# Performance work log

Hardware: AMD Instinct MI355X
Metric: run time of the kernel (lower is better)

The kernel has to match this reference:

```python
import jax, jax.numpy as jnp
import numpy as np

MC = 16384
IND_T = 96
N_MAT = 4
N_STRIKES = 21


def _init_linear(key, fan_in, fan_out, prefix=()):
    k1, k2 = jax.random.split(key)
    lim = 1.0 / np.sqrt(fan_in)
    W = jax.random.uniform(k1, prefix + (fan_in, fan_out), minval=-lim, maxval=lim, dtype=jnp.float32)
    b = jax.random.uniform(k2, prefix + (fan_out,), minval=-lim, maxval=lim, dtype=jnp.float32)
    return W, b


def setup_inputs() -> dict:
    key = jax.random.key(0)
    ks = jax.random.split(key, 14)
    z = jax.random.normal(ks[0], (MC, IND_T), dtype=jnp.float32)
    zz = jax.random.normal(ks[1], (MC, IND_T), dtype=jnp.float32)
    timegrid = jnp.arange(IND_T + 1, dtype=jnp.float32) / 365.0  # daily grid
    maturities = jnp.array([24, 48, 72, 96], dtype=jnp.int32)    # in days
    strikes = jnp.linspace(0.8, 1.2, N_STRIKES, dtype=jnp.float32)
    sv_W1, sv_b1 = _init_linear(ks[2], 3, 100)
    sv_W2, sv_b2 = _init_linear(ks[3], 100, 100)
    sv_W3, sv_b3 = _init_linear(ks[4], 100, 1)
    vh_W1, vh_b1 = _init_linear(ks[5], 2, 20, (N_MAT,))
    vh_W2, vh_b2 = _init_linear(ks[6], 20, N_STRIKES, (N_MAT,))
    vd_W1, vd_b1 = _init_linear(ks[7], 1, 20)
    vd_W2, vd_b2 = _init_linear(ks[8], 20, 1)
    vv_W1, vv_b1 = _init_linear(ks[9], 1, 20)
    vv_W2, vv_b2 = _init_linear(ks[10], 20, 1)
    v0 = jax.random.uniform(ks[11], (1,), dtype=jnp.float32) * 0.1
    rho = jnp.ones((1,), dtype=jnp.float32) * -2.0
    return dict(S0=jnp.float32(1.0), rate=jnp.float32(0.05), z=z, zz=zz,
                timegrid=timegrid, strikes=strikes, v0=v0, rho=rho,
                sv_W1=sv_W1, sv_b1=sv_b1, sv_W2=sv_W2, sv_b2=sv_b2, sv_W3=sv_W3, sv_b3=sv_b3,
                vh_W1=vh_W1, vh_b1=vh_b1, vh_W2=vh_W2, vh_b2=vh_b2,
                vd_W1=vd_W1, vd_b1=vd_b1, vd_W2=vd_W2, vd_b2=vd_b2,
                vv_W1=vv_W1, vv_b1=vv_b1, vv_W2=vv_W2, vv_b2=vv_b2,
                maturities=maturities)


def reference(S0, rate, z, zz, timegrid, strikes, v0, rho,
              sv_W1, sv_b1, sv_W2, sv_b2, sv_W3, sv_b3,
              vh_W1, vh_b1, vh_W2, vh_b2,
              vd_W1, vd_b1, vd_W2, vd_b2,
              vv_W1, vv_b1, vv_W2, vv_b2,
              maturities):
    sg = jax.lax.stop_gradient
    mc = z.shape[0]
    n_mat = vh_W1.shape[0]
    n_strikes = strikes.shape[0]

    def s_vol(x):  # [MC,3] -> [MC,1], softplus output
        h1 = jax.nn.relu(x @ sv_W1 + sv_b1)
        h2 = jax.nn.relu(h1 @ sv_W2 + sv_b2)
        return jax.nn.softplus(h2 @ sv_W3 + sv_b3)

    def v_drift(v):  # [MC,1] -> [MC,1]
        return jax.nn.relu(v @ vd_W1 + vd_b1) @ vd_W2 + vd_b2

    def v_vol(v):  # [MC,1] -> [MC,1], softplus output
        return jax.nn.softplus(jax.nn.relu(v @ vv_W1 + vv_b1) @ vv_W2 + vv_b2)

    def vanilla_hedge_all(x):  # [MC,2] -> [MC, n_strikes, n_mat] (one net per maturity)
        h1 = jax.nn.relu(jnp.einsum('mi,kio->kmo', x, vh_W1) + vh_b1[:, None, :])
        out = jax.nn.softplus(jnp.einsum('kmo,koj->kmj', h1, vh_W2) + vh_b2[:, None, :])
        return jnp.transpose(out, (1, 2, 0))

    rho_t = jnp.tanh(rho)[0]
    days = jnp.round(timegrid * 365.0).astype(jnp.int32)       # [IND_T+1]
    le = days[1:, None] <= maturities[None, :]                  # [IND_T, n_mat]
    idx_net = jnp.argmax(le, axis=1)                            # first live maturity per step
    is_mat = jnp.any(days[1:, None] == maturities[None, :], axis=1)
    mat_idx = jnp.arange(n_mat)

    Slog0 = jnp.log(jnp.full((mc, 1), S0, dtype=jnp.float32))
    V0 = jnp.full((mc, 1), 1.0, dtype=jnp.float32) * jax.nn.sigmoid(v0)[0] * 0.5
    cv0 = jnp.zeros((mc, n_strikes, n_mat), dtype=jnp.float32)
    pv0 = jnp.zeros((n_mat, n_strikes), dtype=jnp.float32)

    xs = (z.T[:, :, None], zz.T[:, :, None], timegrid[:-1], timegrid[1:], idx_net, is_mat)

    def step(carry, x):
        Slog_old, V_old, cv, pv_h, pv_var = carry
        z_i, zz_i, t0, t1, idx, im = x
        h = t1 - t0
        sqh = jnp.sqrt(h)
        dW = sqh * z_i                                          # [MC,1]
        dB = rho_t * dW + jnp.sqrt(1.0 - rho_t ** 2) * sqh * zz_i
        ones_t = jnp.full((mc, 1), 1.0, dtype=jnp.float32) * t0
        pd = s_vol(jnp.concatenate([ones_t, Slog_old, V_old], axis=1))  # price diffusion
        cv_fwd = vanilla_hedge_all(jnp.concatenate([ones_t, sg(Slog_old)], axis=1))
        V_new = V_old + v_drift(V_old) * h + v_vol(V_old) * dB
        drift = rate - 0.5 * pd ** 2
        diff = pd * dW
        drift_c = 1.0 + jnp.abs(sg(drift)) * sqh                # tamed Euler
        diff_c = 1.0 + jnp.abs(sg(pd)) * sqh
        Slog_new = Slog_old + drift * h / drift_c + diff / diff_c
        S_new = jnp.exp(Slog_new)
        S_old = jnp.exp(Slog_old)
        dS = jnp.exp(-rate * t1) * S_new - jnp.exp(-rate * t0) * S_old  # [MC,1]
        mask = (mat_idx >= idx).astype(cv.dtype)                # live maturities only
        cv = cv + mask[None, None, :] * cv_fwd * sg(dS)[:, :, None]
        # hedged vanilla (call) prices collected at maturity steps
        payoff = jnp.exp(-rate * t1) * jnp.maximum(S_new - strikes[None, :], 0.0)
        price = payoff - cv[:, :, idx]                          # [MC, n_strikes]
        pv = jnp.mean(price, axis=0)
        pvar = jnp.var(price, axis=0, ddof=1)
        sel = (mat_idx == idx)[:, None] & im
        pv_h = jnp.where(sel, pv[None, :], pv_h)
        pv_var = jnp.where(sel, pvar[None, :], pv_var)
        return (Slog_new, V_new, cv, pv_h, pv_var), None

    (_, _, _, pv_h, pv_var), _ = jax.lax.scan(step, (Slog0, V0, cv0, pv0, pv0), xs)
    return jnp.stack([pv_h, pv_var])  # [2, n_mat, n_strikes]
```

## Files before the change

kernel.cpp:

```cpp
#include <hip/hip_runtime.h>
#include <hip/hip_bf16.h>
#include <math.h>


#define MC      16384
#define NSTEP   96
#define BLOCK   512
#define NGROUP  512
#define NPAIR   84

typedef short bf16x8 __attribute__((ext_vector_type(8)));
typedef float f32x4  __attribute__((ext_vector_type(4)));

union U8 { uint4 u; bf16x8 v; };
union BF2U { __hip_bfloat162 b; unsigned u; };

__device__ __forceinline__ unsigned bf16rne(float x) {
    unsigned u = __float_as_uint(x);
    return (u + 0x7FFFu + ((u >> 16) & 1u)) >> 16;
}
__device__ __forceinline__ unsigned pk2(float lo, float hi) {
    BF2U t; t.b = __float22bfloat162_rn(make_float2(lo, hi));
    return t.u;
}
__device__ __forceinline__ float sp(float x) {
    return fmaxf(x, 0.f) + __logf(1.f + __expf(-fabsf(x)));
}

__global__ __launch_bounds__(BLOCK, 4)
void lsv_sim(const float* __restrict__ S0p,   const float* __restrict__ ratep,
             const float* __restrict__ z,     const float* __restrict__ zzg,
             const float* __restrict__ strikesg,
             const float* __restrict__ v0p,   const float* __restrict__ rhop,
             const float* __restrict__ svW1,  const float* __restrict__ svb1,
             const float* __restrict__ svW2,  const float* __restrict__ svb2,
             const float* __restrict__ svW3,  const float* __restrict__ svb3,
             const float* __restrict__ vhW1,  const float* __restrict__ vhb1,
             const float* __restrict__ vhW2,  const float* __restrict__ vhb2,
             const float* __restrict__ vdW1,  const float* __restrict__ vdb1,
             const float* __restrict__ vdW2,  const float* __restrict__ vdb2,
             const float* __restrict__ vvW1,  const float* __restrict__ vvb1,
             const float* __restrict__ vvW2,  const float* __restrict__ vvb2,
             const int*   __restrict__ mats,
             float* __restrict__ psum, float* __restrict__ psq)
{
    __shared__ __align__(16) unsigned short H1c[16 * 32 * 8];
    __shared__ __align__(16) float W1f[16 * 32];
    __shared__ __align__(16) float WH1f[16 * 32];
    __shared__ __align__(16) float B2T[128], W3T[128];
    __shared__ __align__(16) float RED[32 * 4];
    __shared__ float VDl[32], VVl[32];
    __shared__ float PSs[2][32], PSq[2][32];
    __shared__ __align__(16) float VW[128];
    __shared__ __align__(16) float4 STEP[NSTEP];
    __shared__ float D1T[NSTEP];
    __shared__ int   ITAB[NSTEP];
    __shared__ float ZT[32][97], ZZT[32][97];
    __shared__ float SLOG[32], VST[32], SST[32], SLOGP[32], DSP[32];
    __shared__ __align__(16) float CW1[2][128];
    __shared__ __align__(16) float CH[2][128];

    const int tid  = threadIdx.x;
    const int lane = tid & 63;
    const int w    = __builtin_amdgcn_readfirstlane(tid >> 6);
    const int quad = lane >> 4;
    const int col  = lane & 15;
    const int lp   = lane & 31;

    const int pt = w & 1;
    const int jg = w >> 1;
    const int hm = w >> 1;

    {
        const size_t gbase = (size_t)blockIdx.x * 32 * NSTEP;
        for (int e = tid; e < 32 * NSTEP; e += BLOCK) {
            const int p = e / NSTEP, ii = e - p * NSTEP;
            ZT[p][ii]  = z  [gbase + e];
            ZZT[p][ii] = zzg[gbase + e];
        }
    }
    for (int e = tid; e < 128; e += BLOCK) {
        float v = 0.f;
        if      (e < 20)             v = vdW1[e];
        else if (e < 40)             v = vdb1[e - 20];
        else if (e < 60)             v = vdW2[e - 40];
        else if (e >= 64 && e < 84)  v = vvW1[e - 64];
        else if (e >= 84 && e < 104) v = vvb1[e - 84];
        else if (e >= 104 && e < 124)v = vvW2[e - 104];
        else if (e == 124)           v = vdb2[0];
        else if (e == 125)           v = vvb2[0];
        VW[e] = v;
        B2T[e] = (e < 100) ? svb2[e] : 0.f;
        W3T[e] = (e < 100) ? svW3[e] : 0.f;
    }
    for (int e = tid; e < 512; e += BLOCK) {
        const int kc2 = e >> 5, r5 = e & 31, grp = r5 >> 3, kk = kc2 * 8 + (r5 & 7);
        float v = 0.f;
        if (kk < 100) v = (grp == 0) ? svW1[kk] : (grp == 1) ? svW1[100 + kk]
                        : (grp == 2) ? svW1[200 + kk] : svb1[kk];
        W1f[e] = v;
    }
    for (int e = tid; e < 512; e += BLOCK) {
        const int hq = e >> 5, r5 = e & 31, grp = r5 >> 3;
        const int hmm = hq >> 2, qq = hq & 3;
        const int j = qq * 8 + (r5 & 7);
        float v = 0.f;
        if (j < 20 && grp < 3)
            v = (grp == 0) ? vhW1[hmm * 40 + j] : (grp == 1) ? vhW1[hmm * 40 + 20 + j]
                                                : vhb1[hmm * 20 + j];
        WH1f[e] = v;
    }

    const float rate  = ratep[0];
    const float S0    = S0p[0];
    const float rho_t = tanhf(rhop[0]);
    const float srho  = sqrtf(1.f - rho_t * rho_t);
    const float b3    = svb3[0];

    if (tid < NSTEP) {
        const int i = tid;
        const float t0 = (float)i       * (1.f / 365.f);
        const float t1 = (float)(i + 1) * (1.f / 365.f);
        const float h  = t1 - t0;
        STEP[i] = make_float4(t0, h, sqrtf(h), __expf(-rate * t0));
        D1T[i]  = __expf(-rate * t1);
        const int day = i + 1;
        const int m0 = mats[0], m1 = mats[1], m2 = mats[2], m3 = mats[3];
        const int idx = (day > m0) + (day > m1) + (day > m2);
        const int mi  = (idx == 0) ? m0 : (idx == 1) ? m1 : (idx == 2) ? m2 : m3;
        ITAB[i] = idx | ((day == mi) ? 256 : 0);
    }

    bf16x8 Af[4][2];
#pragma unroll
    for (int c = 0; c < 4; c++)
#pragma unroll
        for (int t = 0; t < 2; t++) {
            U8 tt;
#pragma unroll
            for (int e2 = 0; e2 < 4; e2++) {
                const int k0 = 32 * c + 8 * quad + 2 * e2;
                const int j  = (2 * jg + t) * 16 + col;
                const float v0 = (k0     < 100 && j < 100) ? svW2[k0 * 100 + j]       : 0.f;
                const float v1 = (k0 + 1 < 100 && j < 100) ? svW2[(k0 + 1) * 100 + j] : 0.f;
                (&tt.u.x)[e2] = bf16rne(v0) | (bf16rne(v1) << 16);
            }
            Af[c][t] = tt.v;
        }
    bf16x8 Ah[2];
#pragma unroll
    for (int st = 0; st < 2; st++) {
        U8 tt;
#pragma unroll
        for (int e2 = 0; e2 < 4; e2++) {
            const int j0 = 8 * quad + 2 * e2, j1 = j0 + 1;
            const int s  = st * 16 + col;
            const float v0 = (j0 < 20 && s < 21) ? vhW2[hm * 420 + j0 * 21 + s] : 0.f;
            const float v1 = (j1 < 20 && s < 21) ? vhW2[hm * 420 + j1 * 21 + s] : 0.f;
            (&tt.u.x)[e2] = bf16rne(v0) | (bf16rne(v1) << 16);
        }
        Ah[st] = tt.v;
    }
    f32x4 c0h, c1h;
    float K0a[4], K1a[4];
#pragma unroll
    for (int r = 0; r < 4; r++) {
        const int s0 = quad * 4 + r, s1 = 16 + quad * 4 + r;
        c0h[r] = vhb2[hm * 21 + s0];
        K0a[r] = strikesg[s0];
        c1h[r] = (s1 < 21) ? vhb2[hm * 21 + s1] : 0.f;
        K1a[r] = (s1 < 21) ? strikesg[s1] : 1e30f;
    }

    float Slog = __logf(S0);
    float S    = __expf(Slog);
    float V    = (1.f / (1.f + __expf(-v0p[0]))) * 0.5f;
    f32x4 cv0 = {0.f, 0.f, 0.f, 0.f};
    f32x4 cv1 = {0.f, 0.f, 0.f, 0.f};

    const int path = pt * 16 + col;
    const int kc   = jg * 4 + quad;

    __syncthreads();

    if (tid < 128) {
        const float t00 = STEP[0].x;
        const int kk = tid;
        CW1[0][kk] = fmaf(t00, W1f[(kk >> 3) * 32 + (kk & 7)],
                               W1f[(kk >> 3) * 32 + 24 + (kk & 7)]);
    } else if (tid < 256) {
        const float t00 = STEP[0].x;
        const int e = tid - 128;
        CH[0][e] = fmaf(t00, WH1f[(e >> 3) * 32 + (e & 7)],
                             WH1f[(e >> 3) * 32 + 16 + (e & 7)]);
    }
    if (tid < 32) {
        SLOG[tid] = Slog;
        SST[tid]  = S;
        VST[tid]  = V;
    }

    __syncthreads();

    const int j0e = (2 * jg) * 16 + quad * 4;
    const float4 b2a = *reinterpret_cast<const float4*>(B2T + j0e);
    const float4 w3a = *reinterpret_cast<const float4*>(W3T + j0e);
    const float4 b2b = *reinterpret_cast<const float4*>(B2T + j0e + 16);
    const float4 w3b = *reinterpret_cast<const float4*>(W3T + j0e + 16);

    auto hedge_step = [&](int ip) {
        const int iv   = ITAB[ip];
        const int idxp = iv & 0xff;
        if (hm >= idxp) {
            const int hb = ip & 1;
            const float slp = SLOGP[path];
            U8 b;
#pragma unroll
            for (int hh = 0; hh < 2; hh++) {
                const float* Wp = WH1f + (hm * 4 + quad) * 32 + 8 + hh * 4;
                const float4 ws4 = *reinterpret_cast<const float4*>(Wp);
                const float4 ch4 = *reinterpret_cast<const float4*>(&CH[hb][(hm * 4 + quad) * 8 + hh * 4]);
                const float x0 = fmaxf(ch4.x + slp * ws4.x, 0.f);
                const float x1 = fmaxf(ch4.y + slp * ws4.y, 0.f);
                const float x2 = fmaxf(ch4.z + slp * ws4.z, 0.f);
                const float x3 = fmaxf(ch4.w + slp * ws4.w, 0.f);
                (&b.u.x)[2 * hh]     = pk2(x0, x1);
                (&b.u.x)[2 * hh + 1] = pk2(x2, x3);
            }
            const f32x4 D0 = __builtin_amdgcn_mfma_f32_16x16x32_bf16(Ah[0], b.v, c0h, 0, 0, 0);
            const f32x4 D1 = __builtin_amdgcn_mfma_f32_16x16x32_bf16(Ah[1], b.v, c1h, 0, 0, 0);
            const float dsP = DSP[path];
#pragma unroll
            for (int r = 0; r < 4; r++) {
                cv0[r] += sp(D0[r]) * dsP;
                cv1[r] += sp(D1[r]) * dsP;
            }
            if ((iv & 256) && hm == idxp) {
                const float Sp  = SST[path];
                const float d1p = D1T[ip];
                float p0[4], q0[4], p1[4], q1[4];
#pragma unroll
                for (int r = 0; r < 4; r++) {
                    p0[r] = d1p * fmaxf(Sp - K0a[r], 0.f) - cv0[r];
                    p1[r] = d1p * fmaxf(Sp - K1a[r], 0.f) - cv1[r];
                    q0[r] = p0[r] * p0[r];
                    q1[r] = p1[r] * p1[r];
                }
#pragma unroll
                for (int o = 1; o <= 8; o <<= 1) {
#pragma unroll
                    for (int r = 0; r < 4; r++) {
                        p0[r] += __shfl_xor(p0[r], o);
                        q0[r] += __shfl_xor(q0[r], o);
                        p1[r] += __shfl_xor(p1[r], o);
                        q1[r] += __shfl_xor(q1[r], o);
                    }
                }
                if (col == 0) {
#pragma unroll
                    for (int r = 0; r < 4; r++) {
                        const int s0 = quad * 4 + r, s1 = 16 + quad * 4 + r;
                        PSs[pt][s0] = p0[r];  PSq[pt][s0] = q0[r];
                        if (s1 < 21) { PSs[pt][s1] = p1[r];  PSq[pt][s1] = q1[r]; }
                    }
                }
            }
        }
    };

    auto ps_reduce = [&](int ip) {
        if (w == 0) {
            const int iv = ITAB[ip];
            if (iv & 256) {
                const int s = lane & 31;
                if (s < 21) {
                    const float* src = (lane >= 32) ? &PSq[0][0] : &PSs[0][0];
                    const float acc = src[s] + src[32 + s];
                    float* dst = (lane >= 32) ? psq : psum;
                    dst[((iv & 0xff) * 21 + s) * NGROUP + blockIdx.x] = acc;
                }
            }
        }
    };

    for (int i = 0; i < NSTEP; i++) {
        const int buf = i & 1;

        {
            const float slp = SLOG[path];
            const float vp  = VST[path];
            const float* Wp = W1f + kc * 32;
            uint4 o;
#pragma unroll
            for (int hh = 0; hh < 2; hh++) {
                const float4 b4 = *reinterpret_cast<const float4*>(Wp + 8 + hh * 4);
                const float4 c4 = *reinterpret_cast<const float4*>(Wp + 16 + hh * 4);
                const float4 cw = *reinterpret_cast<const float4*>(&CW1[buf][kc * 8 + hh * 4]);
                const float x0 = fmaxf(cw.x + slp * b4.x + vp * c4.x, 0.f);
                const float x1 = fmaxf(cw.y + slp * b4.y + vp * c4.y, 0.f);
                const float x2 = fmaxf(cw.z + slp * b4.z + vp * c4.z, 0.f);
                const float x3 = fmaxf(cw.w + slp * b4.w + vp * c4.w, 0.f);
                (&o.x)[2 * hh]     = pk2(x0, x1);
                (&o.x)[2 * hh + 1] = pk2(x2, x3);
            }
            *reinterpret_cast<uint4*>(H1c + (kc * 32 + path) * 8) = o;
        }
        if (i > 0) hedge_step(i - 1);
        if (w == 0) {
            const float Vp = VST[lp];
            const float* bw = VW + ((lane >= 32) ? 64 : 0);
            float a2 = 0.f;
#pragma unroll
            for (int q5 = 0; q5 < 5; q5++) {
                const float4 w1 = *reinterpret_cast<const float4*>(bw + 4 * q5);
                const float4 b1 = *reinterpret_cast<const float4*>(bw + 20 + 4 * q5);
                const float4 w2 = *reinterpret_cast<const float4*>(bw + 40 + 4 * q5);
                a2 += fmaxf(Vp * w1.x + b1.x, 0.f) * w2.x;
                a2 += fmaxf(Vp * w1.y + b1.y, 0.f) * w2.y;
                a2 += fmaxf(Vp * w1.z + b1.z, 0.f) * w2.z;
                a2 += fmaxf(Vp * w1.w + b1.w, 0.f) * w2.w;
            }
            if (lane < 32) VDl[lp] = a2; else VVl[lp] = a2;
        }
        __syncthreads();

        {
            f32x4 d0 = {0.f, 0.f, 0.f, 0.f};
            f32x4 d1 = {0.f, 0.f, 0.f, 0.f};
#pragma unroll
            for (int c = 0; c < 4; c++) {
                const bf16x8 b = *reinterpret_cast<const bf16x8*>(
                    H1c + ((quad + 4 * c) * 32 + path) * 8);
                d0 = __builtin_amdgcn_mfma_f32_16x16x32_bf16(Af[c][0], b, d0, 0, 0, 0);
                d1 = __builtin_amdgcn_mfma_f32_16x16x32_bf16(Af[c][1], b, d1, 0, 0, 0);
            }
            float acc = fmaxf(d0[0] + b2a.x, 0.f) * w3a.x
                      + fmaxf(d0[1] + b2a.y, 0.f) * w3a.y
                      + fmaxf(d0[2] + b2a.z, 0.f) * w3a.z
                      + fmaxf(d0[3] + b2a.w, 0.f) * w3a.w
                      + fmaxf(d1[0] + b2b.x, 0.f) * w3b.x
                      + fmaxf(d1[1] + b2b.y, 0.f) * w3b.y
                      + fmaxf(d1[2] + b2b.z, 0.f) * w3b.z
                      + fmaxf(d1[3] + b2b.w, 0.f) * w3b.w;
            acc += __shfl_xor(acc, 16);
            acc += __shfl_xor(acc, 32);
            if (quad == 0)
                RED[path * 4 + jg] = acc;
        }
        if (i > 0) ps_reduce(i - 1);
        __syncthreads();

        if (w == 1) {
            const float4 rr = *reinterpret_cast<const float4*>(RED + lp * 4);
            const float pout = (rr.x + rr.y) + (rr.z + rr.w);
            const float pd = sp(pout + b3);
            const float vdv = VDl[lp] + VW[124];
            const float vvv = sp(VVl[lp] + VW[125]);
            const float4 u  = STEP[i];
            const float sqh = u.z;
            const float zi  = ZT[lp][i];
            const float zzi = ZZT[lp][i];
            const float dW = sqh * zi;
            const float dB = rho_t * dW + srho * sqh * zzi;
            const float Vn = V + vdv * u.y + vvv * dB;
            const float drift   = rate - 0.5f * pd * pd;
            const float diff    = pd * dW;
            const float drift_c = 1.f + fabsf(drift) * sqh;
            const float diff_c  = 1.f + fabsf(pd) * sqh;
            const float Sln = Slog + __fdividef(drift * u.y, drift_c) + __fdividef(diff, diff_c);
            const float Sn  = __expf(Sln);
            const float dS  = D1T[i] * Sn - u.w * S;
            if (lane < 32) {
                SLOGP[lp] = Slog;  DSP[lp] = dS;
                SLOG[lp]  = Sln;   SST[lp] = Sn;  VST[lp] = Vn;
            }
            Slog = Sln; S = Sn; V = Vn;
        } else if ((w == 2 || w == 3) && i + 1 < NSTEP) {
            const float t0n = STEP[i + 1].x;
            const int kk = (w - 2) * 64 + lane;
            CW1[buf ^ 1][kk] = fmaf(t0n, W1f[(kk >> 3) * 32 + (kk & 7)],
                                         W1f[(kk >> 3) * 32 + 24 + (kk & 7)]);
        } else if ((w == 4 || w == 5) && i + 1 < NSTEP) {
            const float t0n = STEP[i + 1].x;
            const int e = (w - 4) * 64 + lane;
            CH[buf ^ 1][e] = fmaf(t0n, WH1f[(e >> 3) * 32 + (e & 7)],
                                       WH1f[(e >> 3) * 32 + 16 + (e & 7)]);
        }
        __syncthreads();
    }

    hedge_step(NSTEP - 1);
    __syncthreads();
    ps_reduce(NSTEP - 1);
}

__global__ void lsv_finalize(const float* __restrict__ psum,
                             const float* __restrict__ psq,
                             float* __restrict__ out)
{
    const int t    = blockIdx.x;
    const int lane = threadIdx.x;
    float s = 0.f, q = 0.f;
    for (int b = lane; b < NGROUP; b += 64) {
        s += psum[t * NGROUP + b];
        q += psq [t * NGROUP + b];
    }
#pragma unroll
    for (int o = 1; o <= 32; o <<= 1) {
        s += __shfl_xor(s, o);
        q += __shfl_xor(q, o);
    }
    if (lane == 0) {
        const float mean = s * (1.0f / (float)MC);
        const float var  = (q - (float)MC * mean * mean) * (1.0f / (float)(MC - 1));
        out[t]         = mean;
        out[NPAIR + t] = var;
    }
}

extern "C" void kernel_launch(void* const* d_in, const int* in_sizes, int n_in,
                              void* d_out, int out_size, void* d_ws, size_t ws_size,
                              hipStream_t stream)
{
    const float* S0    = (const float*)d_in[0];
    const float* rate  = (const float*)d_in[1];
    const float* z     = (const float*)d_in[2];
    const float* zz    = (const float*)d_in[3];
    const float* strikes = (const float*)d_in[5];
    const float* v0    = (const float*)d_in[6];
    const float* rho   = (const float*)d_in[7];
    const float* svW1  = (const float*)d_in[8];
    const float* svb1  = (const float*)d_in[9];
    const float* svW2  = (const float*)d_in[10];
    const float* svb2  = (const float*)d_in[11];
    const float* svW3  = (const float*)d_in[12];
    const float* svb3  = (const float*)d_in[13];
    const float* vhW1  = (const float*)d_in[14];
    const float* vhb1  = (const float*)d_in[15];
    const float* vhW2  = (const float*)d_in[16];
    const float* vhb2  = (const float*)d_in[17];
    const float* vdW1  = (const float*)d_in[18];
    const float* vdb1  = (const float*)d_in[19];
    const float* vdW2  = (const float*)d_in[20];
    const float* vdb2  = (const float*)d_in[21];
    const float* vvW1  = (const float*)d_in[22];
    const float* vvb1  = (const float*)d_in[23];
    const float* vvW2  = (const float*)d_in[24];
    const float* vvb2  = (const float*)d_in[25];
    const int*   mats  = (const int*)d_in[26];

    float* psum = (float*)d_ws;
    float* psq  = psum + NPAIR * NGROUP;

    hipLaunchKernelGGL(lsv_sim, dim3(NGROUP), dim3(BLOCK), 0, stream,
                       S0, rate, z, zz, strikes, v0, rho,
                       svW1, svb1, svW2, svb2, svW3, svb3,
                       vhW1, vhb1, vhW2, vhb2,
                       vdW1, vdb1, vdW2, vdb2,
                       vvW1, vvb1, vvW2, vvb2,
                       mats, psum, psq);

    hipLaunchKernelGGL(lsv_finalize, dim3(NPAIR), dim3(64), 0, stream,
                       psum, psq, (float*)d_out);
}
```

Before: 392.3 us.

## Replicate per-path state update in every wave to remove a barrier per step

The SDE state update (Slog, S, V, dS) used to run only in wave 1 and be shared through LDS, which cost an extra __syncthreads each step. Now every wave recomputes it redundantly for its own path, reading RED and double-buffered VD/VV arrays, so the barrier and the shared state arrays go away. The hedge MFMA is issued before the state update to overlap with it, and the local-vol MLP now runs in two waves with double buffering. The cost is redundant scalar math in all eight waves and higher register pressure.

```diff
diff --git a/kernel.cpp b/kernel.cpp
--- a/kernel.cpp
+++ b/kernel.cpp
@@ -49,14 +49,13 @@
     __shared__ __align__(16) float WH1f[16 * 32];
     __shared__ __align__(16) float B2T[128], W3T[128];
     __shared__ __align__(16) float RED[32 * 4];
-    __shared__ float VDl[32], VVl[32];
+    __shared__ float VDb[2][32], VVb[2][32];
     __shared__ float PSs[2][32], PSq[2][32];
     __shared__ __align__(16) float VW[128];
     __shared__ __align__(16) float4 STEP[NSTEP];
     __shared__ float D1T[NSTEP];
     __shared__ int   ITAB[NSTEP];
     __shared__ float ZT[32][97], ZZT[32][97];
-    __shared__ float SLOG[32], VST[32], SST[32], SLOGP[32], DSP[32];
     __shared__ __align__(16) float CW1[2][128];
     __shared__ __align__(16) float CH[2][128];
 
@@ -65,11 +64,12 @@
     const int w    = __builtin_amdgcn_readfirstlane(tid >> 6);
     const int quad = lane >> 4;
     const int col  = lane & 15;
-    const int lp   = lane & 31;
 
     const int pt = w & 1;
     const int jg = w >> 1;
     const int hm = w >> 1;
+    const int path = pt * 16 + col;
+    const int kc   = jg * 4 + quad;
 
     {
         const size_t gbase = (size_t)blockIdx.x * 32 * NSTEP;
@@ -177,9 +177,7 @@
     float V    = (1.f / (1.f + __expf(-v0p[0]))) * 0.5f;
     f32x4 cv0 = {0.f, 0.f, 0.f, 0.f};
     f32x4 cv1 = {0.f, 0.f, 0.f, 0.f};
-
-    const int path = pt * 16 + col;
-    const int kc   = jg * 4 + quad;
+    float Slog_prev = 0.f, dS_prev = 0.f;
 
     __syncthreads();
 
@@ -194,11 +192,6 @@
         CH[0][e] = fmaf(t00, WH1f[(e >> 3) * 32 + (e & 7)],
                              WH1f[(e >> 3) * 32 + 16 + (e & 7)]);
     }
-    if (tid < 32) {
-        SLOG[tid] = Slog;
-        SST[tid]  = S;
-        VST[tid]  = V;
-    }
 
     __syncthreads();
 
@@ -207,65 +200,31 @@
     const float4 w3a = *reinterpret_cast<const float4*>(W3T + j0e);
     const float4 b2b = *reinterpret_cast<const float4*>(B2T + j0e + 16);
     const float4 w3b = *reinterpret_cast<const float4*>(W3T + j0e + 16);
-
-    auto hedge_step = [&](int ip) {
-        const int iv   = ITAB[ip];
-        const int idxp = iv & 0xff;
-        if (hm >= idxp) {
-            const int hb = ip & 1;
-            const float slp = SLOGP[path];
-            U8 b;
-#pragma unroll
-            for (int hh = 0; hh < 2; hh++) {
-                const float* Wp = WH1f + (hm * 4 + quad) * 32 + 8 + hh * 4;
-                const float4 ws4 = *reinterpret_cast<const float4*>(Wp);
-                const float4 ch4 = *reinterpret_cast<const float4*>(&CH[hb][(hm * 4 + quad) * 8 + hh * 4]);
-                const float x0 = fmaxf(ch4.x + slp * ws4.x, 0.f);
-                const float x1 = fmaxf(ch4.y + slp * ws4.y, 0.f);
-                const float x2 = fmaxf(ch4.z + slp * ws4.z, 0.f);
-                const float x3 = fmaxf(ch4.w + slp * ws4.w, 0.f);
-                (&b.u.x)[2 * hh]     = pk2(x0, x1);
-                (&b.u.x)[2 * hh + 1] = pk2(x2, x3);
-            }
-            const f32x4 D0 = __builtin_amdgcn_mfma_f32_16x16x32_bf16(Ah[0], b.v, c0h, 0, 0, 0);
-            const f32x4 D1 = __builtin_amdgcn_mfma_f32_16x16x32_bf16(Ah[1], b.v, c1h, 0, 0, 0);
-            const float dsP = DSP[path];
-#pragma unroll
-            for (int r = 0; r < 4; r++) {
-                cv0[r] += sp(D0[r]) * dsP;
-                cv1[r] += sp(D1[r]) * dsP;
-            }
-            if ((iv & 256) && hm == idxp) {
-                const float Sp  = SST[path];
-                const float d1p = D1T[ip];
-                float p0[4], q0[4], p1[4], q1[4];
-#pragma unroll
-                for (int r = 0; r < 4; r++) {
-                    p0[r] = d1p * fmaxf(Sp - K0a[r], 0.f) - cv0[r];
-                    p1[r] = d1p * fmaxf(Sp - K1a[r], 0.f) - cv1[r];
-                    q0[r] = p0[r] * p0[r];
-                    q1[r] = p1[r] * p1[r];
-                }
-#pragma unroll
-                for (int o = 1; o <= 8; o <<= 1) {
-#pragma unroll
-                    for (int r = 0; r < 4; r++) {
-                        p0[r] += __shfl_xor(p0[r], o);
-                        q0[r] += __shfl_xor(q0[r], o);
-                        p1[r] += __shfl_xor(p1[r], o);
-                        q1[r] += __shfl_xor(q1[r], o);
-                    }
-                }
-                if (col == 0) {
-#pragma unroll
-                    for (int r = 0; r < 4; r++) {
-                        const int s0 = quad * 4 + r, s1 = 16 + quad * 4 + r;
-                        PSs[pt][s0] = p0[r];  PSq[pt][s0] = q0[r];
-                        if (s1 < 21) { PSs[pt][s1] = p1[r];  PSq[pt][s1] = q1[r]; }
-                    }
-                }
-            }
-        }
+    const float4 wsA = *reinterpret_cast<const float4*>(WH1f + (hm * 4 + quad) * 32 + 8);
+    const float4 wsB = *reinterpret_cast<const float4*>(WH1f + (hm * 4 + quad) * 32 + 12);
+
+    auto r3 = [&](int i) {
+        const float4 rr = *reinterpret_cast<const float4*>(RED + path * 4);
+        const float pout = (rr.x + rr.y) + (rr.z + rr.w);
+        const float pd  = sp(pout + b3);
+        const float vdv = VDb[i & 1][path] + VW[124];
+        const float vvv = sp(VVb[i & 1][path] + VW[125]);
+        const float4 u  = STEP[i];
+        const float sqh = u.z;
+        const float zi  = ZT[path][i];
+        const float zzi = ZZT[path][i];
+        const float dW = sqh * zi;
+        const float dB = rho_t * dW + srho * sqh * zzi;
+        const float Vn = V + vdv * u.y + vvv * dB;
+        const float drift   = rate - 0.5f * pd * pd;
+        const float diff    = pd * dW;
+        const float drift_c = 1.f + fabsf(drift) * sqh;
+        const float diff_c  = 1.f + fabsf(pd) * sqh;
+        const float Sln = Slog + __fdividef(drift * u.y, drift_c) + __fdividef(diff, diff_c);
+        const float Sn  = __expf(Sln);
+        const float dS  = D1T[i] * Sn - u.w * S;
+        Slog_prev = Slog; dS_prev = dS;
+        Slog = Sln; S = Sn; V = Vn;
     };
 
     auto ps_reduce = [&](int ip) {
@@ -286,9 +245,45 @@
     for (int i = 0; i < NSTEP; i++) {
         const int buf = i & 1;
 
+        f32x4 spD0, spD1;
+        bool hact = false;
+        int  ivp  = 0;
+        if (i > 0) {
+            ivp  = ITAB[i - 1];
+            hact = (hm >= (ivp & 0xff));
+            if (hact) {
+                const int hb = (i - 1) & 1;
+                const float slp = Slog;
+                U8 b;
+                {
+                    const float4 ch4 = *reinterpret_cast<const float4*>(&CH[hb][(hm * 4 + quad) * 8]);
+                    (&b.u.x)[0] = pk2(fmaxf(ch4.x + slp * wsA.x, 0.f),
+                                      fmaxf(ch4.y + slp * wsA.y, 0.f));
+                    (&b.u.x)[1] = pk2(fmaxf(ch4.z + slp * wsA.z, 0.f),
+                                      fmaxf(ch4.w + slp * wsA.w, 0.f));
+                }
+                {
+                    const float4 ch4 = *reinterpret_cast<const float4*>(&CH[hb][(hm * 4 + quad) * 8 + 4]);
+                    (&b.u.x)[2] = pk2(fmaxf(ch4.x + slp * wsB.x, 0.f),
+                                      fmaxf(ch4.y + slp * wsB.y, 0.f));
+                    (&b.u.x)[3] = pk2(fmaxf(ch4.z + slp * wsB.z, 0.f),
+                                      fmaxf(ch4.w + slp * wsB.w, 0.f));
+                }
+                const f32x4 D0 = __builtin_amdgcn_mfma_f32_16x16x32_bf16(Ah[0], b.v, c0h, 0, 0, 0);
+                const f32x4 D1 = __builtin_amdgcn_mfma_f32_16x16x32_bf16(Ah[1], b.v, c1h, 0, 0, 0);
+#pragma unroll
+                for (int r = 0; r < 4; r++) {
+                    spD0[r] = sp(D0[r]);
+                    spD1[r] = sp(D1[r]);
+                }
+            }
+        }
+
+        if (i > 0) r3(i - 1);
+
         {
-            const float slp = SLOG[path];
-            const float vp  = VST[path];
+            const float slp = Slog;
+            const float vp  = V;
             const float* Wp = W1f + kc * 32;
             uint4 o;
 #pragma unroll
@@ -305,9 +300,47 @@
             }
             *reinterpret_cast<uint4*>(H1c + (kc * 32 + path) * 8) = o;
         }
-        if (i > 0) hedge_step(i - 1);
-        if (w == 0) {
-            const float Vp = VST[lp];
+
+        if (hact) {
+#pragma unroll
+            for (int r = 0; r < 4; r++) {
+                cv0[r] += spD0[r] * dS_prev;
+                cv1[r] += spD1[r] * dS_prev;
+            }
+            if ((ivp & 256) && hm == (ivp & 0xff)) {
+                const float Sp  = S;
+                const float d1p = D1T[i - 1];
+                float p0[4], q0[4], p1[4], q1[4];
+#pragma unroll
+                for (int r = 0; r < 4; r++) {
+                    p0[r] = d1p * fmaxf(Sp - K0a[r], 0.f) - cv0[r];
+                    p1[r] = d1p * fmaxf(Sp - K1a[r], 0.f) - cv1[r];
+                    q0[r] = p0[r] * p0[r];
+                    q1[r] = p1[r] * p1[r];
+                }
+#pragma unroll
+                for (int o = 1; o <= 8; o <<= 1) {
+#pragma unroll
+                    for (int r = 0; r < 4; r++) {
+                        p0[r] += __shfl_xor(p0[r], o);
+                        q0[r] += __shfl_xor(q0[r], o);
+                        p1[r] += __shfl_xor(p1[r], o);
+                        q1[r] += __shfl_xor(q1[r], o);
+                    }
+                }
+                if (col == 0) {
+#pragma unroll
+                    for (int r = 0; r < 4; r++) {
+                        const int s0 = quad * 4 + r, s1 = 16 + quad * 4 + r;
+                        PSs[pt][s0] = p0[r];  PSq[pt][s0] = q0[r];
+                        if (s1 < 21) { PSs[pt][s1] = p1[r];  PSq[pt][s1] = q1[r]; }
+                    }
+                }
+            }
+        }
+
+        if (w < 2) {
+            const float Vp = V;
             const float* bw = VW + ((lane >= 32) ? 64 : 0);
             float a2 = 0.f;
 #pragma unroll
@@ -320,7 +353,8 @@
                 a2 += fmaxf(Vp * w1.z + b1.z, 0.f) * w2.z;
                 a2 += fmaxf(Vp * w1.w + b1.w, 0.f) * w2.w;
             }
-            if (lane < 32) VDl[lp] = a2; else VVl[lp] = a2;
+            if (quad == 0)      VDb[buf][path] = a2;
+            else if (quad == 2) VVb[buf][path] = a2;
         }
         __syncthreads();
 
@@ -348,34 +382,7 @@
                 RED[path * 4 + jg] = acc;
         }
         if (i > 0) ps_reduce(i - 1);
-        __syncthreads();
-
-        if (w == 1) {
-            const float4 rr = *reinterpret_cast<const float4*>(RED + lp * 4);
-            const float pout = (rr.x + rr.y) + (rr.z + rr.w);
-            const float pd = sp(pout + b3);
-            const float vdv = VDl[lp] + VW[124];
-            const float vvv = sp(VVl[lp] + VW[125]);
-            const float4 u  = STEP[i];
-            const float sqh = u.z;
-            const float zi  = ZT[lp][i];
-            const float zzi = ZZT[lp][i];
-            const float dW = sqh * zi;
-            const float dB = rho_t * dW + srho * sqh * zzi;
-            const float Vn = V + vdv * u.y + vvv * dB;
-            const float drift   = rate - 0.5f * pd * pd;
-            const float diff    = pd * dW;
-            const float drift_c = 1.f + fabsf(drift) * sqh;
-            const float diff_c  = 1.f + fabsf(pd) * sqh;
-            const float Sln = Slog + __fdividef(drift * u.y, drift_c) + __fdividef(diff, diff_c);
-            const float Sn  = __expf(Sln);
-            const float dS  = D1T[i] * Sn - u.w * S;
-            if (lane < 32) {
-                SLOGP[lp] = Slog;  DSP[lp] = dS;
-                SLOG[lp]  = Sln;   SST[lp] = Sn;  VST[lp] = Vn;
-            }
-            Slog = Sln; S = Sn; V = Vn;
-        } else if ((w == 2 || w == 3) && i + 1 < NSTEP) {
+        if ((w == 2 || w == 3) && i + 1 < NSTEP) {
             const float t0n = STEP[i + 1].x;
             const int kk = (w - 2) * 64 + lane;
             CW1[buf ^ 1][kk] = fmaf(t0n, W1f[(kk >> 3) * 32 + (kk & 7)],
@@ -389,7 +396,75 @@
         __syncthreads();
     }
 
-    hedge_step(NSTEP - 1);
+    {
+        const int ivp = ITAB[NSTEP - 1];
+        const bool hact = (hm >= (ivp & 0xff));
+        f32x4 spD0, spD1;
+        if (hact) {
+            const int hb = (NSTEP - 1) & 1;
+            const float slp = Slog;
+            U8 b;
+            {
+                const float4 ch4 = *reinterpret_cast<const float4*>(&CH[hb][(hm * 4 + quad) * 8]);
+                (&b.u.x)[0] = pk2(fmaxf(ch4.x + slp * wsA.x, 0.f),
+                                  fmaxf(ch4.y + slp * wsA.y, 0.f));
+                (&b.u.x)[1] = pk2(fmaxf(ch4.z + slp * wsA.z, 0.f),
+                                  fmaxf(ch4.w + slp * wsA.w, 0.f));
+            }
+            {
+                const float4 ch4 = *reinterpret_cast<const float4*>(&CH[hb][(hm * 4 + quad) * 8 + 4]);
+                (&b.u.x)[2] = pk2(fmaxf(ch4.x + slp * wsB.x, 0.f),
+                                  fmaxf(ch4.y + slp * wsB.y, 0.f));
+                (&b.u.x)[3] = pk2(fmaxf(ch4.z + slp * wsB.z, 0.f),
+                                  fmaxf(ch4.w + slp * wsB.w, 0.f));
+            }
+            const f32x4 D0 = __builtin_amdgcn_mfma_f32_16x16x32_bf16(Ah[0], b.v, c0h, 0, 0, 0);
+            const f32x4 D1 = __builtin_amdgcn_mfma_f32_16x16x32_bf16(Ah[1], b.v, c1h, 0, 0, 0);
+#pragma unroll
+            for (int r = 0; r < 4; r++) {
+                spD0[r] = sp(D0[r]);
+                spD1[r] = sp(D1[r]);
+            }
+        }
+        r3(NSTEP - 1);
+        if (hact) {
+#pragma unroll
+            for (int r = 0; r < 4; r++) {
+                cv0[r] += spD0[r] * dS_prev;
+                cv1[r] += spD1[r] * dS_prev;
+            }
+            if ((ivp & 256) && hm == (ivp & 0xff)) {
+                const float Sp  = S;
+                const float d1p = D1T[NSTEP - 1];
+                float p0[4], q0[4], p1[4], q1[4];
+#pragma unroll
+                for (int r = 0; r < 4; r++) {
+                    p0[r] = d1p * fmaxf(Sp - K0a[r], 0.f) - cv0[r];
+                    p1[r] = d1p * fmaxf(Sp - K1a[r], 0.f) - cv1[r];
+                    q0[r] = p0[r] * p0[r];
+                    q1[r] = p1[r] * p1[r];
+                }
+#pragma unroll
+                for (int o = 1; o <= 8; o <<= 1) {
+#pragma unroll
+                    for (int r = 0; r < 4; r++) {
+                        p0[r] += __shfl_xor(p0[r], o);
+                        q0[r] += __shfl_xor(q0[r], o);
+                        p1[r] += __shfl_xor(p1[r], o);
+                        q1[r] += __shfl_xor(q1[r], o);
+                    }
+                }
+                if (col == 0) {
+#pragma unroll
+                    for (int r = 0; r < 4; r++) {
+                        const int s0 = quad * 4 + r, s1 = 16 + quad * 4 + r;
+                        PSs[pt][s0] = p0[r];  PSq[pt][s0] = q0[r];
+                        if (s1 < 21) { PSs[pt][s1] = p1[r];  PSq[pt][s1] = q1[r]; }
+                    }
+                }
+            }
+        }
+    }
     __syncthreads();
     ps_reduce(NSTEP - 1);
 }
```

Measured after the change: 435.5 us. +11.0%, slower.

## Halve block to 16 paths and 4 waves, doubling block count

Applied to the files above, without the earlier changes.

Each block now simulates 16 Monte Carlo paths with 4 waves instead of 32 paths with 8 waves, so the grid doubles to 1024 groups. Each wave owns one hidden-column group and one maturity hedge, and the per-step state (Slog, S, V) is read from shared memory instead of per-thread registers. The goal is more resident blocks and cheaper barriers across the 96 serial steps. The cost is that the cross-pair partial-sum reduction goes away while the finalize kernel must reduce twice as many partials, and MFMA tiles use only half their columns per block.

```diff
diff --git a/kernel.cpp b/kernel.cpp
--- a/kernel.cpp
+++ b/kernel.cpp
@@ -5,8 +5,8 @@
 
 #define MC      16384
 #define NSTEP   96
-#define BLOCK   512
-#define NGROUP  512
+#define BLOCK   256
+#define NGROUP  1024
 #define NPAIR   84
 
 typedef short bf16x8 __attribute__((ext_vector_type(8)));
@@ -44,19 +44,19 @@
              const int*   __restrict__ mats,
              float* __restrict__ psum, float* __restrict__ psq)
 {
-    __shared__ __align__(16) unsigned short H1c[16 * 32 * 8];
+    __shared__ __align__(16) unsigned short H1c[16 * 16 * 8];
     __shared__ __align__(16) float W1f[16 * 32];
     __shared__ __align__(16) float WH1f[16 * 32];
     __shared__ __align__(16) float B2T[128], W3T[128];
-    __shared__ __align__(16) float RED[32 * 4];
-    __shared__ float VDl[32], VVl[32];
-    __shared__ float PSs[2][32], PSq[2][32];
+    __shared__ __align__(16) float RED[16 * 4];
+    __shared__ float VDb[16], VVb[16];
+    __shared__ float PSs[32], PSq[32];
     __shared__ __align__(16) float VW[128];
     __shared__ __align__(16) float4 STEP[NSTEP];
     __shared__ float D1T[NSTEP];
     __shared__ int   ITAB[NSTEP];
-    __shared__ float ZT[32][97], ZZT[32][97];
-    __shared__ float SLOG[32], VST[32], SST[32], SLOGP[32], DSP[32];
+    __shared__ float ZT[16][97], ZZT[16][97];
+    __shared__ float SLOG[16], VST[16], SST[16], SLOGP[16], DSP[16];
     __shared__ __align__(16) float CW1[2][128];
     __shared__ __align__(16) float CH[2][128];
 
@@ -65,15 +65,14 @@
     const int w    = __builtin_amdgcn_readfirstlane(tid >> 6);
     const int quad = lane >> 4;
     const int col  = lane & 15;
-    const int lp   = lane & 31;
-
-    const int pt = w & 1;
-    const int jg = w >> 1;
-    const int hm = w >> 1;
+
+    const int hm   = w;
+    const int path = col;
+    const int kc   = w * 4 + quad;
 
     {
-        const size_t gbase = (size_t)blockIdx.x * 32 * NSTEP;
-        for (int e = tid; e < 32 * NSTEP; e += BLOCK) {
+        const size_t gbase = (size_t)blockIdx.x * 16 * NSTEP;
+        for (int e = tid; e < 16 * NSTEP; e += BLOCK) {
             const int p = e / NSTEP, ii = e - p * NSTEP;
             ZT[p][ii]  = z  [gbase + e];
             ZZT[p][ii] = zzg[gbase + e];
@@ -140,7 +139,7 @@
 #pragma unroll
             for (int e2 = 0; e2 < 4; e2++) {
                 const int k0 = 32 * c + 8 * quad + 2 * e2;
-                const int j  = (2 * jg + t) * 16 + col;
+                const int j  = (2 * w + t) * 16 + col;
                 const float v0 = (k0     < 100 && j < 100) ? svW2[k0 * 100 + j]       : 0.f;
                 const float v1 = (k0 + 1 < 100 && j < 100) ? svW2[(k0 + 1) * 100 + j] : 0.f;
                 (&tt.u.x)[e2] = bf16rne(v0) | (bf16rne(v1) << 16);
@@ -172,14 +171,11 @@
         K1a[r] = (s1 < 21) ? strikesg[s1] : 1e30f;
     }
 
-    float Slog = __logf(S0);
-    float S    = __expf(Slog);
-    float V    = (1.f / (1.f + __expf(-v0p[0]))) * 0.5f;
+    const float Slog0 = __logf(S0);
+    const float S0v   = __expf(Slog0);
+    const float V0v   = (1.f / (1.f + __expf(-v0p[0]))) * 0.5f;
     f32x4 cv0 = {0.f, 0.f, 0.f, 0.f};
     f32x4 cv1 = {0.f, 0.f, 0.f, 0.f};
-
-    const int path = pt * 16 + col;
-    const int kc   = jg * 4 + quad;
 
     __syncthreads();
 
@@ -188,25 +184,27 @@
         const int kk = tid;
         CW1[0][kk] = fmaf(t00, W1f[(kk >> 3) * 32 + (kk & 7)],
                                W1f[(kk >> 3) * 32 + 24 + (kk & 7)]);
-    } else if (tid < 256) {
+    } else {
         const float t00 = STEP[0].x;
         const int e = tid - 128;
         CH[0][e] = fmaf(t00, WH1f[(e >> 3) * 32 + (e & 7)],
                              WH1f[(e >> 3) * 32 + 16 + (e & 7)]);
     }
-    if (tid < 32) {
-        SLOG[tid] = Slog;
-        SST[tid]  = S;
-        VST[tid]  = V;
+    if (tid < 16) {
+        SLOG[tid] = Slog0;
+        SST[tid]  = S0v;
+        VST[tid]  = V0v;
     }
 
     __syncthreads();
 
-    const int j0e = (2 * jg) * 16 + quad * 4;
+    const int j0e = (2 * w) * 16 + quad * 4;
     const float4 b2a = *reinterpret_cast<const float4*>(B2T + j0e);
     const float4 w3a = *reinterpret_cast<const float4*>(W3T + j0e);
     const float4 b2b = *reinterpret_cast<const float4*>(B2T + j0e + 16);
     const float4 w3b = *reinterpret_cast<const float4*>(W3T + j0e + 16);
+    const float4 wsA = *reinterpret_cast<const float4*>(WH1f + (hm * 4 + quad) * 32 + 8);
+    const float4 wsB = *reinterpret_cast<const float4*>(WH1f + (hm * 4 + quad) * 32 + 12);
 
     auto hedge_step = [&](int ip) {
         const int iv   = ITAB[ip];
@@ -215,17 +213,19 @@
             const int hb = ip & 1;
             const float slp = SLOGP[path];
             U8 b;
-#pragma unroll
-            for (int hh = 0; hh < 2; hh++) {
-                const float* Wp = WH1f + (hm * 4 + quad) * 32 + 8 + hh * 4;
-                const float4 ws4 = *reinterpret_cast<const float4*>(Wp);
-                const float4 ch4 = *reinterpret_cast<const float4*>(&CH[hb][(hm * 4 + quad) * 8 + hh * 4]);
-                const float x0 = fmaxf(ch4.x + slp * ws4.x, 0.f);
-                const float x1 = fmaxf(ch4.y + slp * ws4.y, 0.f);
-                const float x2 = fmaxf(ch4.z + slp * ws4.z, 0.f);
-                const float x3 = fmaxf(ch4.w + slp * ws4.w, 0.f);
-                (&b.u.x)[2 * hh]     = pk2(x0, x1);
-                (&b.u.x)[2 * hh + 1] = pk2(x2, x3);
+            {
+                const float4 ch4 = *reinterpret_cast<const float4*>(&CH[hb][(hm * 4 + quad) * 8]);
+                (&b.u.x)[0] = pk2(fmaxf(ch4.x + slp * wsA.x, 0.f),
+                                  fmaxf(ch4.y + slp * wsA.y, 0.f));
+                (&b.u.x)[1] = pk2(fmaxf(ch4.z + slp * wsA.z, 0.f),
+                                  fmaxf(ch4.w + slp * wsA.w, 0.f));
+            }
+            {
+                const float4 ch4 = *reinterpret_cast<const float4*>(&CH[hb][(hm * 4 + quad) * 8 + 4]);
+                (&b.u.x)[2] = pk2(fmaxf(ch4.x + slp * wsB.x, 0.f),
+                                  fmaxf(ch4.y + slp * wsB.y, 0.f));
+                (&b.u.x)[3] = pk2(fmaxf(ch4.z + slp * wsB.z, 0.f),
+                                  fmaxf(ch4.w + slp * wsB.w, 0.f));
             }
             const f32x4 D0 = __builtin_amdgcn_mfma_f32_16x16x32_bf16(Ah[0], b.v, c0h, 0, 0, 0);
             const f32x4 D1 = __builtin_amdgcn_mfma_f32_16x16x32_bf16(Ah[1], b.v, c1h, 0, 0, 0);
@@ -260,8 +260,8 @@
 #pragma unroll
                     for (int r = 0; r < 4; r++) {
                         const int s0 = quad * 4 + r, s1 = 16 + quad * 4 + r;
-                        PSs[pt][s0] = p0[r];  PSq[pt][s0] = q0[r];
-                        if (s1 < 21) { PSs[pt][s1] = p1[r];  PSq[pt][s1] = q1[r]; }
+                        PSs[s0] = p0[r];  PSq[s0] = q0[r];
+                        if (s1 < 21) { PSs[s1] = p1[r];  PSq[s1] = q1[r]; }
                     }
                 }
             }
@@ -274,8 +274,8 @@
             if (iv & 256) {
                 const int s = lane & 31;
                 if (s < 21) {
-                    const float* src = (lane >= 32) ? &PSq[0][0] : &PSs[0][0];
-                    const float acc = src[s] + src[32 + s];
+                    const float* src = (lane >= 32) ? &PSq[0] : &PSs[0];
+                    const float acc = src[s];
                     float* dst = (lane >= 32) ? psq : psum;
                     dst[((iv & 0xff) * 21 + s) * NGROUP + blockIdx.x] = acc;
                 }
@@ -303,11 +303,11 @@
                 (&o.x)[2 * hh]     = pk2(x0, x1);
                 (&o.x)[2 * hh + 1] = pk2(x2, x3);
             }
-            *reinterpret_cast<uint4*>(H1c + (kc * 32 + path) * 8) = o;
+            *reinterpret_cast<uint4*>(H1c + (kc * 16 + path) * 8) = o;
         }
         if (i > 0) hedge_step(i - 1);
-        if (w == 0) {
-            const float Vp = VST[lp];
+        if (w == 1) {
+            const float Vp = VST[path];
             const float* bw = VW + ((lane >= 32) ? 64 : 0);
             float a2 = 0.f;
 #pragma unroll
@@ -320,7 +320,8 @@
                 a2 += fmaxf(Vp * w1.z + b1.z, 0.f) * w2.z;
                 a2 += fmaxf(Vp * w1.w + b1.w, 0.f) * w2.w;
             }
-            if (lane < 32) VDl[lp] = a2; else VVl[lp] = a2;
+            if (quad == 0)      VDb[path] = a2;
+            else if (quad == 2) VVb[path] = a2;
         }
         __syncthreads();
 
@@ -330,7 +331,7 @@
 #pragma unroll
             for (int c = 0; c < 4; c++) {
                 const bf16x8 b = *reinterpret_cast<const bf16x8*>(
-                    H1c + ((quad + 4 * c) * 32 + path) * 8);
+                    H1c + ((quad + 4 * c) * 16 + path) * 8);
                 d0 = __builtin_amdgcn_mfma_f32_16x16x32_bf16(Af[c][0], b, d0, 0, 0, 0);
                 d1 = __builtin_amdgcn_mfma_f32_16x16x32_bf16(Af[c][1], b, d1, 0, 0, 0);
             }
@@ -345,46 +346,55 @@
             acc += __shfl_xor(acc, 16);
             acc += __shfl_xor(acc, 32);
             if (quad == 0)
-                RED[path * 4 + jg] = acc;
+                RED[path * 4 + w] = acc;
         }
         if (i > 0) ps_reduce(i - 1);
         __syncthreads();
 
-        if (w == 1) {
+        if (w == 0) {
+            const int lp = lane & 15;
             const float4 rr = *reinterpret_cast<const float4*>(RED + lp * 4);
             const float pout = (rr.x + rr.y) + (rr.z + rr.w);
             const float pd = sp(pout + b3);
-            const float vdv = VDl[lp] + VW[124];
-            const float vvv = sp(VVl[lp] + VW[125]);
+            const float vdv = VDb[lp] + VW[124];
+            const float vvv = sp(VVb[lp] + VW[125]);
             const float4 u  = STEP[i];
             const float sqh = u.z;
             const float zi  = ZT[lp][i];
             const float zzi = ZZT[lp][i];
             const float dW = sqh * zi;
             const float dB = rho_t * dW + srho * sqh * zzi;
-            const float Vn = V + vdv * u.y + vvv * dB;
+            const float Vold = VST[lp];
+            const float Sold = SST[lp];
+            const float SlogO = SLOG[lp];
+            const float Vn = Vold + vdv * u.y + vvv * dB;
             const float drift   = rate - 0.5f * pd * pd;
             const float diff    = pd * dW;
             const float drift_c = 1.f + fabsf(drift) * sqh;
             const float diff_c  = 1.f + fabsf(pd) * sqh;
-            const float Sln = Slog + __fdividef(drift * u.y, drift_c) + __fdividef(diff, diff_c);
+            const float Sln = SlogO + __fdividef(drift * u.y, drift_c) + __fdividef(diff, diff_c);
             const float Sn  = __expf(Sln);
-            const float dS  = D1T[i] * Sn - u.w * S;
-            if (lane < 32) {
-                SLOGP[lp] = Slog;  DSP[lp] = dS;
-                SLOG[lp]  = Sln;   SST[lp] = Sn;  VST[lp] = Vn;
-            }
-            Slog = Sln; S = Sn; V = Vn;
-        } else if ((w == 2 || w == 3) && i + 1 < NSTEP) {
+            const float dS  = D1T[i] * Sn - u.w * Sold;
+            if (lane < 16) {
+                SLOGP[lp] = SlogO;  DSP[lp] = dS;
+                SLOG[lp]  = Sln;    SST[lp] = Sn;  VST[lp] = Vn;
+            }
+        } else if (w == 2 && i + 1 < NSTEP) {
             const float t0n = STEP[i + 1].x;
-            const int kk = (w - 2) * 64 + lane;
-            CW1[buf ^ 1][kk] = fmaf(t0n, W1f[(kk >> 3) * 32 + (kk & 7)],
-                                         W1f[(kk >> 3) * 32 + 24 + (kk & 7)]);
-        } else if ((w == 4 || w == 5) && i + 1 < NSTEP) {
+#pragma unroll
+            for (int rep = 0; rep < 2; rep++) {
+                const int kk = rep * 64 + lane;
+                CW1[buf ^ 1][kk] = fmaf(t0n, W1f[(kk >> 3) * 32 + (kk & 7)],
+                                             W1f[(kk >> 3) * 32 + 24 + (kk & 7)]);
+            }
+        } else if (w == 3 && i + 1 < NSTEP) {
             const float t0n = STEP[i + 1].x;
-            const int e = (w - 4) * 64 + lane;
-            CH[buf ^ 1][e] = fmaf(t0n, WH1f[(e >> 3) * 32 + (e & 7)],
-                                       WH1f[(e >> 3) * 32 + 16 + (e & 7)]);
+#pragma unroll
+            for (int rep = 0; rep < 2; rep++) {
+                const int e = rep * 64 + lane;
+                CH[buf ^ 1][e] = fmaf(t0n, WH1f[(e >> 3) * 32 + (e & 7)],
+                                           WH1f[(e >> 3) * 32 + 16 + (e & 7)]);
+            }
         }
         __syncthreads();
     }
```

After: 455.8 us. +16.2%, slower.
